# Kernel tuning notes

Hardware: AMD Instinct MI355X
Metric: run time of the kernel (lower is better)

Reference implementation:

```python
import jax, jax.numpy as jnp
import numpy as np

D_MODEL = 512
D_FFN = 2048
N_LAYERS = 6
VOCAB = 1000
D_STATE = 16
D_CONV = 4
D_INNER = 2 * D_MODEL  # expand=2
DT_RANK = 32           # ceil(d_model/16)
B, LT, LS = 2, 512, 512


def _pos_encoding(length, d_model):
    pos = np.arange(length, dtype=np.float32)[:, None]
    div = np.exp(np.arange(0, d_model, 2, dtype=np.float32) * (-np.log(10000.0) / d_model))
    pe = np.zeros((length, d_model), np.float32)
    pe[:, 0::2] = np.sin(pos * div)
    pe[:, 1::2] = np.cos(pos * div)
    return jnp.asarray(pe)


def _layer_norm(x, g, b, eps=1e-6):
    m = x.mean(-1, keepdims=True)
    v = ((x - m) ** 2).mean(-1, keepdims=True)
    return (x - m) * jax.lax.rsqrt(v + eps) * g + b


def _mamba(x, in_w, conv_w, conv_b, xproj_w, dt_w, dt_b, A_log, Dskip, out_w):
    # x: (b, l, d_model)
    b, l, _ = x.shape
    xz = x @ in_w.T                                   # (b, l, 2*d_inner)
    xc, z = jnp.split(xz, 2, axis=-1)
    # causal depthwise conv over time
    xt = jnp.transpose(xc, (0, 2, 1))                 # (b, d_inner, l)
    xt = jnp.pad(xt, ((0, 0), (0, 0), (D_CONV - 1, 0)))
    xt = jax.lax.conv_general_dilated(
        xt, conv_w, window_strides=(1,), padding='VALID',
        feature_group_count=D_INNER, dimension_numbers=('NCH', 'OIH', 'NCH'))
    xc = jax.nn.silu(jnp.transpose(xt, (0, 2, 1)) + conv_b)  # (b, l, d_inner)
    dbl = xc @ xproj_w.T                              # (b, l, dt_rank + 2*n)
    dt, Bm, Cm = jnp.split(dbl, [DT_RANK, DT_RANK + D_STATE], axis=-1)
    dt = jax.nn.softplus(dt @ dt_w.T + dt_b)          # (b, l, d_inner)
    A = -jnp.exp(A_log)                               # (d_inner, n)

    def step(h, xs):
        dt_t, B_t, C_t, u_t = xs                      # (b,d),(b,n),(b,n),(b,d)
        dA = jnp.exp(dt_t[..., None] * A)             # (b, d, n)
        h = dA * h + (dt_t * u_t)[..., None] * B_t[:, None, :]
        y = jnp.einsum('bdn,bn->bd', h, C_t)
        return h, y

    h0 = jnp.zeros((b, D_INNER, D_STATE), x.dtype)
    xs = (jnp.swapaxes(dt, 0, 1), jnp.swapaxes(Bm, 0, 1),
          jnp.swapaxes(Cm, 0, 1), jnp.swapaxes(xc, 0, 1))
    _, ys = jax.lax.scan(step, h0, xs)                # ys: (l, b, d_inner)
    y = jnp.swapaxes(ys, 0, 1) + xc * Dskip
    y = y * jax.nn.silu(z)
    return y @ out_w.T                                # (b, l, d_model)


def setup_inputs() -> dict:
    key = jax.random.key(0)
    ks = iter(jax.random.split(key, 40))

    def rn(shape, s=0.02):
        return jax.random.normal(next(ks), shape, jnp.float32) * s

    def mamba_params():
        return dict(
            in_w=rn((N_LAYERS, 2 * D_INNER, D_MODEL)),
            conv_w=rn((N_LAYERS, D_INNER, 1, D_CONV), 0.1),
            conv_b=rn((N_LAYERS, D_INNER)),
            xproj=rn((N_LAYERS, DT_RANK + 2 * D_STATE, D_INNER)),
            dtw=rn((N_LAYERS, D_INNER, DT_RANK)),
            dtb=rn((N_LAYERS, D_INNER)),
            Alog=jnp.log(jnp.broadcast_to(jnp.arange(1.0, D_STATE + 1.0, dtype=jnp.float32), (N_LAYERS, D_INNER, D_STATE))),
            D=jnp.ones((N_LAYERS, D_INNER), jnp.float32),
            outw=rn((N_LAYERS, D_MODEL, D_INNER)),
        )

    ps, pc = mamba_params(), mamba_params()
    inp = {
        'src': jax.random.normal(next(ks), (B, LS, D_MODEL), jnp.float32),
        'tgt': jax.random.randint(next(ks), (B, LT), 0, VOCAB),
        'emb': rn((VOCAB, D_MODEL)),
        'in_w_s': ps['in_w'], 'conv_w_s': ps['conv_w'], 'conv_b_s': ps['conv_b'],
        'xproj_s': ps['xproj'], 'dtw_s': ps['dtw'], 'dtb_s': ps['dtb'],
        'Alog_s': ps['Alog'], 'D_s': ps['D'], 'outw_s': ps['outw'],
        'in_w_c': pc['in_w'], 'conv_w_c': pc['conv_w'], 'conv_b_c': pc['conv_b'],
        'xproj_c': pc['xproj'], 'dtw_c': pc['dtw'], 'dtb_c': pc['dtb'],
        'Alog_c': pc['Alog'], 'D_c': pc['D'], 'outw_c': pc['outw'],
        'ffn_w1': rn((N_LAYERS, D_FFN, D_MODEL)),
        'ffn_b1': jnp.zeros((N_LAYERS, D_FFN), jnp.float32),
        'ffn_w2': rn((N_LAYERS, D_MODEL, D_FFN)),
        'ffn_b2': jnp.zeros((N_LAYERS, D_MODEL), jnp.float32),
        'ln_g': jnp.ones((N_LAYERS, 3, D_MODEL), jnp.float32),
        'ln_b': jnp.zeros((N_LAYERS, 3, D_MODEL), jnp.float32),
        'fin_g': jnp.ones((D_MODEL,), jnp.float32),
        'fin_b': jnp.zeros((D_MODEL,), jnp.float32),
    }
    return inp


def reference(src, tgt, emb, in_w_s, conv_w_s, conv_b_s, xproj_s, dtw_s, dtb_s,
              Alog_s, D_s, outw_s, in_w_c, conv_w_c, conv_b_c, xproj_c, dtw_c,
              dtb_c, Alog_c, D_c, outw_c, ffn_w1, ffn_b1, ffn_w2, ffn_b2,
              ln_g, ln_b, fin_g, fin_b):
    # NormalizedEmbedding + sinusoidal positional encoding
    x = emb[tgt] * jnp.sqrt(jnp.asarray(D_MODEL, jnp.float32))
    x = x + _pos_encoding(LT, D_MODEL)[None]
    for i in range(N_LAYERS):
        # self mamba (post-norm, normalize_before=False)
        t2 = _mamba(x, in_w_s[i], conv_w_s[i], conv_b_s[i], xproj_s[i],
                    dtw_s[i], dtb_s[i], Alog_s[i], D_s[i], outw_s[i])
        x = _layer_norm(x + t2, ln_g[i, 0], ln_b[i, 0])
        # cross mamba over concat([memory, tgt]) then take last LT steps
        cat = jnp.concatenate([src, x], axis=1)
        t2 = _mamba(cat, in_w_c[i], conv_w_c[i], conv_b_c[i], xproj_c[i],
                    dtw_c[i], dtb_c[i], Alog_c[i], D_c[i], outw_c[i])[:, -LT:]
        x = _layer_norm(x + t2, ln_g[i, 1], ln_b[i, 1])
        # positionwise FFN
        h = jax.nn.relu(x @ ffn_w1[i].T + ffn_b1[i]) @ ffn_w2[i].T + ffn_b2[i]
        x = _layer_norm(x + h, ln_g[i, 2], ln_b[i, 2])
    return _layer_norm(x, fin_g, fin_b)
```

## Files before the change

kernel.cpp:

```cpp
#include <hip/hip_runtime.h>
#include <math.h>

#define DMODEL 512
#define DINNER 1024
#define DSTATE 16
#define DTRANK 32
#define NLAYERS 6
#define BB 2
#define LT 512
#define LS 512

typedef __attribute__((ext_vector_type(8))) short bf16x8;
typedef __attribute__((ext_vector_type(8))) unsigned short u16x8;
typedef __attribute__((ext_vector_type(4))) float f32x4;

__device__ __forceinline__ unsigned short f2bf(float f) {
  unsigned u = __float_as_uint(f);
  u += 0x7fffu + ((u >> 16) & 1u);
  return (unsigned short)(u >> 16);
}
__device__ __forceinline__ float bf2f(unsigned short u) {
  return __uint_as_float((unsigned)u << 16);
}

template<int EPI>
__device__ __forceinline__ float epi_apply(float acc, float b) {
  if (EPI == 1) { float v = acc + b; return v > 0.f ? v : 0.f; }
  if (EPI == 2) { return acc + b; }
  if (EPI == 3) { float v = acc + b; return fmaxf(v, 0.f) + log1pf(__expf(-fabsf(v))); }
  return acc;
}

__global__ __launch_bounds__(256) void cvt_all_kernel(
    const float* __restrict__ i0, const float* __restrict__ i1,
    const float* __restrict__ i2, const float* __restrict__ i3,
    const float* __restrict__ i4, const float* __restrict__ i5,
    const float* __restrict__ i6, const float* __restrict__ i7,
    const float* __restrict__ i8, const float* __restrict__ i9,
    unsigned short* __restrict__ outbase) {
  int i = blockIdx.x * 256 + threadIdx.x;
  if (i >= 8159232) return;
  const float* in; int off;
  if      (i < 1572864) { in = i0; off = i; }
  else if (i < 3145728) { in = i1; off = i - 1572864; }
  else if (i < 3244032) { in = i2; off = i - 3145728; }
  else if (i < 3342336) { in = i3; off = i - 3244032; }
  else if (i < 3391488) { in = i4; off = i - 3342336; }
  else if (i < 3440640) { in = i5; off = i - 3391488; }
  else if (i < 4227072) { in = i6; off = i - 3440640; }
  else if (i < 5013504) { in = i7; off = i - 4227072; }
  else if (i < 6586368) { in = i8; off = i - 5013504; }
  else                  { in = i9; off = i - 6586368; }
  float4 a = ((const float4*)in)[off];
  ushort4 o = make_ushort4(f2bf(a.x), f2bf(a.y), f2bf(a.z), f2bf(a.w));
  *(ushort4*)&outbase[(size_t)i * 4] = o;
}

__global__ __launch_bounds__(256) void embed_kernel(const int* __restrict__ tgt,
    const float* __restrict__ emb, float* __restrict__ X,
    unsigned short* __restrict__ Xb) {
  int i = blockIdx.x * 256 + threadIdx.x;
  int d = i & (DMODEL - 1);
  int bt = i >> 9;
  int t = bt & (LT - 1);
  int tok = tgt[bt];
  float div = __expf((float)(d & ~1) * (-9.210340371976184f / (float)DMODEL));
  float ang = (float)t * div;
  float pe = (d & 1) ? cosf(ang) : sinf(ang);
  float v = emb[(size_t)tok * DMODEL + d] * 22.627416997969522f + pe;
  X[i] = v;
  Xb[i] = f2bf(v);
}

__global__ __launch_bounds__(256) void catsrc_kernel(const float* __restrict__ src,
    unsigned short* __restrict__ CATb) {
  int i = blockIdx.x * 256 + threadIdx.x;
  int c8 = (i & 63) * 8;
  int r = i >> 6;
  int b = r >> 9, l = r & 511;
  const float* s = src + ((size_t)b * 512 + l) * DMODEL + c8;
  float4 a = *(const float4*)s;
  float4 bq = *(const float4*)(s + 4);
  u16x8 o;
  o[0] = f2bf(a.x); o[1] = f2bf(a.y); o[2] = f2bf(a.z); o[3] = f2bf(a.w);
  o[4] = f2bf(bq.x); o[5] = f2bf(bq.y); o[6] = f2bf(bq.z); o[7] = f2bf(bq.w);
  *(u16x8*)&CATb[((size_t)b * 1024 + l) * DMODEL + c8] = o;
}

template<int BK, int EPI, bool SPLIT, bool OUTB>
__global__ __launch_bounds__(256) void mgemmA(
    const unsigned short* __restrict__ A, const unsigned short* __restrict__ Bw,
    const float* __restrict__ bias, float* __restrict__ C,
    unsigned short* __restrict__ Cb, int M, int N, int K, int lda) {
  constexpr int PAD = BK + 8;
  constexpr int CHA = BK / 32;
  constexpr int CHB = BK / 16;
  __shared__ __align__(16) unsigned short As[64 * PAD];
  __shared__ __align__(16) unsigned short Bs[128 * PAD];
  const int tid = threadIdx.x;
  const int bn = blockIdx.x * 128;
  const int bm = blockIdx.y * 64;
  const int lane = tid & 63;
  const int w = tid >> 6;
  const int wr = (w >> 1) * 32;
  const int wc = (w & 1) * 64;
  const int l15 = lane & 15;
  const int l4 = lane >> 4;
  const int koff = l4 * 8;
  int kcnt = K, kbeg = 0;
  if (SPLIT) { kcnt = K / (int)gridDim.z; kbeg = blockIdx.z * kcnt; }
  const int nt = kcnt / BK;
  f32x4 acc[2][4] = {};

  int arow_[CHA], ak8_[CHA];
  const unsigned short* Ap[CHA];
#pragma unroll
  for (int i = 0; i < CHA; ++i) {
    int f = tid + 256 * i;
    arow_[i] = f / (BK / 8);
    ak8_[i] = (f % (BK / 8)) * 8;
    Ap[i] = A + (size_t)(bm + arow_[i]) * lda + kbeg + ak8_[i];
  }
  int brow_[CHB], bk8_[CHB];
  const unsigned short* Bp[CHB];
#pragma unroll
  for (int i = 0; i < CHB; ++i) {
    int f = tid + 256 * i;
    brow_[i] = f / (BK / 8);
    bk8_[i] = (f % (BK / 8)) * 8;
    Bp[i] = Bw + (size_t)(bn + brow_[i]) * K + kbeg + bk8_[i];
  }

  u16x8 av[CHA], bv[CHB];
#pragma unroll
  for (int i = 0; i < CHA; ++i) av[i] = *(const u16x8*)Ap[i];
#pragma unroll
  for (int i = 0; i < CHB; ++i) bv[i] = *(const u16x8*)Bp[i];

  for (int t = 0; t < nt; ++t) {
    __syncthreads();
#pragma unroll
    for (int i = 0; i < CHA; ++i) *(u16x8*)&As[arow_[i] * PAD + ak8_[i]] = av[i];
#pragma unroll
    for (int i = 0; i < CHB; ++i) *(u16x8*)&Bs[brow_[i] * PAD + bk8_[i]] = bv[i];
    if (t + 1 < nt) {
      int ko = (t + 1) * BK;
#pragma unroll
      for (int i = 0; i < CHA; ++i) av[i] = *(const u16x8*)(Ap[i] + ko);
#pragma unroll
      for (int i = 0; i < CHB; ++i) bv[i] = *(const u16x8*)(Bp[i] + ko);
    }
    __syncthreads();
#pragma unroll
    for (int kk = 0; kk < BK / 32; ++kk) {
      bf16x8 afr[2], bfr[4];
#pragma unroll
      for (int i = 0; i < 2; ++i)
        afr[i] = *(const bf16x8*)&As[(wr + i * 16 + l15) * PAD + kk * 32 + koff];
#pragma unroll
      for (int j = 0; j < 4; ++j)
        bfr[j] = *(const bf16x8*)&Bs[(wc + j * 16 + l15) * PAD + kk * 32 + koff];
#pragma unroll
      for (int fr = 0; fr < 2; ++fr)
#pragma unroll
        for (int fc = 0; fc < 4; ++fc)
          acc[fr][fc] = __builtin_amdgcn_mfma_f32_16x16x32_bf16(
              afr[fr], bfr[fc], acc[fr][fc], 0, 0, 0);
    }
  }

  if (SPLIT) {
    float* Pz = C + (size_t)blockIdx.z * M * N;
#pragma unroll
    for (int fc = 0; fc < 4; ++fc) {
      int col = bn + wc + fc * 16 + l15;
#pragma unroll
      for (int fr = 0; fr < 2; ++fr) {
        int row0 = bm + wr + fr * 16 + l4 * 4;
#pragma unroll
        for (int r = 0; r < 4; ++r)
          Pz[(size_t)(row0 + r) * N + col] = acc[fr][fc][r];
      }
    }
  } else {
#pragma unroll
    for (int fc = 0; fc < 4; ++fc) {
      int col = bn + wc + fc * 16 + l15;
      float bvs = (EPI != 0) ? bias[col] : 0.f;
#pragma unroll
      for (int fr = 0; fr < 2; ++fr) {
        int row0 = bm + wr + fr * 16 + l4 * 4;
#pragma unroll
        for (int r = 0; r < 4; ++r) {
          float v = epi_apply<EPI>(acc[fr][fc][r], bvs);
          if (OUTB) Cb[(size_t)(row0 + r) * N + col] = f2bf(v);
          else      C[(size_t)(row0 + r) * N + col] = v;
        }
      }
    }
  }
}

template<int BK, int EPI, bool SPLIT, bool OUTB>
__global__ __launch_bounds__(256) void mgemm(
    const unsigned short* __restrict__ A, const unsigned short* __restrict__ Bw,
    const float* __restrict__ bias, float* __restrict__ C,
    unsigned short* __restrict__ Cb, int M, int N, int K, int lda) {
  constexpr int PAD = BK + 8;
  constexpr int CH = BK / 32;
  __shared__ __align__(16) unsigned short As[64 * PAD];
  __shared__ __align__(16) unsigned short Bs[64 * PAD];
  const int tid = threadIdx.x;
  const int bn = blockIdx.x * 64;
  const int bm = blockIdx.y * 64;
  const int lane = tid & 63;
  const int w = tid >> 6;
  const int wr = (w >> 1) * 32;
  const int wc = (w & 1) * 32;
  const int l15 = lane & 15;
  const int l4 = lane >> 4;
  const int koff = l4 * 8;
  int kcnt = K, kbeg = 0;
  if (SPLIT) { kcnt = K / (int)gridDim.z; kbeg = blockIdx.z * kcnt; }
  const int nt = kcnt / BK;
  f32x4 acc[2][2] = {};

  int row_[CH], k8_[CH];
  const unsigned short *Ap[CH], *Bp[CH];
#pragma unroll
  for (int i = 0; i < CH; ++i) {
    int f = tid + 256 * i;
    row_[i] = f / (BK / 8);
    k8_[i] = (f % (BK / 8)) * 8;
    Ap[i] = A + (size_t)(bm + row_[i]) * lda + kbeg + k8_[i];
    Bp[i] = Bw + (size_t)(bn + row_[i]) * K + kbeg + k8_[i];
  }

  u16x8 av[CH], bv[CH];
#pragma unroll
  for (int i = 0; i < CH; ++i) { av[i] = *(const u16x8*)Ap[i]; bv[i] = *(const u16x8*)Bp[i]; }

  for (int t = 0; t < nt; ++t) {
    __syncthreads();
#pragma unroll
    for (int i = 0; i < CH; ++i) {
      *(u16x8*)&As[row_[i] * PAD + k8_[i]] = av[i];
      *(u16x8*)&Bs[row_[i] * PAD + k8_[i]] = bv[i];
    }
    if (t + 1 < nt) {
      int ko = (t + 1) * BK;
#pragma unroll
      for (int i = 0; i < CH; ++i) {
        av[i] = *(const u16x8*)(Ap[i] + ko);
        bv[i] = *(const u16x8*)(Bp[i] + ko);
      }
    }
    __syncthreads();
#pragma unroll
    for (int kk = 0; kk < CH; ++kk) {
      bf16x8 afr[2], bfr[2];
#pragma unroll
      for (int i = 0; i < 2; ++i) {
        afr[i] = *(const bf16x8*)&As[(wr + i * 16 + l15) * PAD + kk * 32 + koff];
        bfr[i] = *(const bf16x8*)&Bs[(wc + i * 16 + l15) * PAD + kk * 32 + koff];
      }
#pragma unroll
      for (int fr = 0; fr < 2; ++fr)
#pragma unroll
        for (int fc = 0; fc < 2; ++fc)
          acc[fr][fc] = __builtin_amdgcn_mfma_f32_16x16x32_bf16(
              afr[fr], bfr[fc], acc[fr][fc], 0, 0, 0);
    }
  }

  if (SPLIT) {
    float* Pz = C + (size_t)blockIdx.z * M * N;
#pragma unroll
    for (int fc = 0; fc < 2; ++fc) {
      int col = bn + wc + fc * 16 + l15;
#pragma unroll
      for (int fr = 0; fr < 2; ++fr) {
        int row0 = bm + wr + fr * 16 + l4 * 4;
#pragma unroll
        for (int r = 0; r < 4; ++r)
          Pz[(size_t)(row0 + r) * N + col] = acc[fr][fc][r];
      }
    }
  } else {
#pragma unroll
    for (int fc = 0; fc < 2; ++fc) {
      int col = bn + wc + fc * 16 + l15;
      float bvs = (EPI != 0) ? bias[col] : 0.f;
#pragma unroll
      for (int fr = 0; fr < 2; ++fr) {
        int row0 = bm + wr + fr * 16 + l4 * 4;
#pragma unroll
        for (int r = 0; r < 4; ++r) {
          float v = epi_apply<EPI>(acc[fr][fc][r], bvs);
          if (OUTB) Cb[(size_t)(row0 + r) * N + col] = f2bf(v);
          else      C[(size_t)(row0 + r) * N + col] = v;
        }
      }
    }
  }
}

__global__ __launch_bounds__(256) void mgemm_dt(
    const float* __restrict__ XPP, const unsigned short* __restrict__ Bw,
    const float* __restrict__ bias, unsigned short* __restrict__ Cb,
    int M, int N) {
  constexpr int PAD = 40;
  __shared__ __align__(16) unsigned short As[64 * PAD];
  __shared__ __align__(16) unsigned short Bs[64 * PAD];
  const int tid = threadIdx.x;
  const int bn = blockIdx.x * 64;
  const int bm = blockIdx.y * 64;
  const int lane = tid & 63;
  const int w = tid >> 6;
  const int wr = (w >> 1) * 32;
  const int wc = (w & 1) * 32;
  const int l15 = lane & 15;
  const int l4 = lane >> 4;
  const int koff = l4 * 8;
  const size_t zs = (size_t)M * 64;
  {
    int r = tid >> 2, c8 = (tid & 3) * 8;
    const float* p = XPP + (size_t)(bm + r) * 64 + c8;
    float s[8] = {0.f, 0.f, 0.f, 0.f, 0.f, 0.f, 0.f, 0.f};
#pragma unroll
    for (int z = 0; z < 8; ++z) {
      float4 a = *(const float4*)(p + z * zs);
      float4 b = *(const float4*)(p + z * zs + 4);
      s[0] += a.x; s[1] += a.y; s[2] += a.z; s[3] += a.w;
      s[4] += b.x; s[5] += b.y; s[6] += b.z; s[7] += b.w;
    }
    u16x8 o;
#pragma unroll
    for (int j = 0; j < 8; ++j) o[j] = f2bf(s[j]);
    *(u16x8*)&As[r * PAD + c8] = o;
    *(u16x8*)&Bs[r * PAD + c8] = *(const u16x8*)(Bw + (size_t)(bn + r) * 32 + c8);
  }
  __syncthreads();
  bf16x8 afr[2], bfr[2];
#pragma unroll
  for (int i = 0; i < 2; ++i) {
    afr[i] = *(const bf16x8*)&As[(wr + i * 16 + l15) * PAD + koff];
    bfr[i] = *(const bf16x8*)&Bs[(wc + i * 16 + l15) * PAD + koff];
  }
  f32x4 acc[2][2] = {};
#pragma unroll
  for (int fr = 0; fr < 2; ++fr)
#pragma unroll
    for (int fc = 0; fc < 2; ++fc)
      acc[fr][fc] = __builtin_amdgcn_mfma_f32_16x16x32_bf16(
          afr[fr], bfr[fc], acc[fr][fc], 0, 0, 0);
#pragma unroll
  for (int fc = 0; fc < 2; ++fc) {
    int col = bn + wc + fc * 16 + l15;
    float bvs = bias[col];
#pragma unroll
    for (int fr = 0; fr < 2; ++fr) {
      int row0 = bm + wr + fr * 16 + l4 * 4;
#pragma unroll
      for (int r = 0; r < 4; ++r)
        Cb[(size_t)(row0 + r) * N + col] = f2bf(epi_apply<3>(acc[fr][fc][r], bvs));
    }
  }
}

__global__ __launch_bounds__(256) void conv_silu_kernel(
    const unsigned short* __restrict__ xzb, const float* __restrict__ w,
    const float* __restrict__ bias, unsigned short* __restrict__ outb, int L) {
  int idx = blockIdx.x * 256 + threadIdx.x;
  int d8 = (idx & 127) * 8;
  int bt = idx >> 7;
  int b = bt / L;
  int t = bt - b * L;
  const unsigned short* col = xzb + ((size_t)b * L) * (2 * DINNER) + d8;
  float acc[8];
  float4 wv[8];
#pragma unroll
  for (int j = 0; j < 8; ++j) {
    acc[j] = bias[d8 + j];
    wv[j] = *(const float4*)(w + (size_t)(d8 + j) * 4);
  }
#pragma unroll
  for (int k = 0; k < 4; ++k) {
    int tt = t - 3 + k;
    if (tt >= 0) {
      u16x8 v = *(const u16x8*)(col + (size_t)tt * (2 * DINNER));
      float wk[8] = {
        k == 0 ? wv[0].x : k == 1 ? wv[0].y : k == 2 ? wv[0].z : wv[0].w,
        k == 0 ? wv[1].x : k == 1 ? wv[1].y : k == 2 ? wv[1].z : wv[1].w,
        k == 0 ? wv[2].x : k == 1 ? wv[2].y : k == 2 ? wv[2].z : wv[2].w,
        k == 0 ? wv[3].x : k == 1 ? wv[3].y : k == 2 ? wv[3].z : wv[3].w,
        k == 0 ? wv[4].x : k == 1 ? wv[4].y : k == 2 ? wv[4].z : wv[4].w,
        k == 0 ? wv[5].x : k == 1 ? wv[5].y : k == 2 ? wv[5].z : wv[5].w,
        k == 0 ? wv[6].x : k == 1 ? wv[6].y : k == 2 ? wv[6].z : wv[6].w,
        k == 0 ? wv[7].x : k == 1 ? wv[7].y : k == 2 ? wv[7].z : wv[7].w };
#pragma unroll
      for (int j = 0; j < 8; ++j) acc[j] = fmaf(bf2f(v[j]), wk[j], acc[j]);
    }
  }
  u16x8 o;
#pragma unroll
  for (int j = 0; j < 8; ++j) {
    float sig = 1.f / (1.f + __expf(-acc[j]));
    o[j] = f2bf(acc[j] * sig);
  }
  *(u16x8*)&outb[(size_t)bt * DINNER + d8] = o;
}

__global__ __launch_bounds__(256) void scan_pass1(
    const unsigned short* __restrict__ dt, const float* __restrict__ XPP,
    const unsigned short* __restrict__ u, const float* __restrict__ Alog,
    float* __restrict__ P, float* __restrict__ S, int L, int CL) {
  __shared__ float BC[32][32];
  const int tid = threadIdx.x;
  const int d = blockIdx.x * 256 + tid;
  const int b = blockIdx.y;
  const int c = blockIdx.z;
  const int t0 = c * CL;
  if (tid < CL * 4) {
    int t = tid >> 2, j8 = (tid & 3) * 8;
    const float* p = XPP + ((size_t)b * L + t0 + t) * 64 + 32 + j8;
    const size_t zs = (size_t)BB * L * 64;
    float s[8] = {0.f, 0.f, 0.f, 0.f, 0.f, 0.f, 0.f, 0.f};
#pragma unroll
    for (int z = 0; z < 8; ++z) {
      float4 a = *(const float4*)(p + z * zs);
      float4 bq = *(const float4*)(p + z * zs + 4);
      s[0] += a.x; s[1] += a.y; s[2] += a.z; s[3] += a.w;
      s[4] += bq.x; s[5] += bq.y; s[6] += bq.z; s[7] += bq.w;
    }
#pragma unroll
    for (int j = 0; j < 8; ++j) BC[t][j8 + j] = s[j];
  }
  float A[16], h[16], Pp[16];
#pragma unroll
  for (int j = 0; j < 4; ++j) {
    float4 a4 = *(const float4*)(Alog + d * 16 + j * 4);
    A[j * 4 + 0] = -__expf(a4.x); A[j * 4 + 1] = -__expf(a4.y);
    A[j * 4 + 2] = -__expf(a4.z); A[j * 4 + 3] = -__expf(a4.w);
  }
#pragma unroll
  for (int n = 0; n < 16; ++n) { h[n] = 0.f; Pp[n] = 1.f; }
  const unsigned short* dtp = dt + ((size_t)b * L + t0) * DINNER + d;
  const unsigned short* up  = u  + ((size_t)b * L + t0) * DINNER + d;
  __syncthreads();
  float dtv = bf2f(dtp[0]), uv = bf2f(up[0]);
  for (int t = 0; t < CL; ++t) {
    float dtn = 0.f, un = 0.f;
    if (t + 1 < CL) {
      dtn = bf2f(dtp[(size_t)(t + 1) * DINNER]);
      un  = bf2f(up[(size_t)(t + 1) * DINNER]);
    }
    float du = dtv * uv;
#pragma unroll
    for (int n = 0; n < 16; ++n) {
      float dA = __expf(dtv * A[n]);
      Pp[n] *= dA;
      h[n] = fmaf(dA, h[n], du * BC[t][n]);
    }
    dtv = dtn; uv = un;
  }
  size_t base = (size_t)c * 32768 + ((size_t)(b * 1024 + d) << 4);
#pragma unroll
  for (int j = 0; j < 4; ++j) {
    *(float4*)&P[base + j * 4] = make_float4(Pp[j*4], Pp[j*4+1], Pp[j*4+2], Pp[j*4+3]);
    *(float4*)&S[base + j * 4] = make_float4(h[j*4], h[j*4+1], h[j*4+2], h[j*4+3]);
  }
}

__global__ __launch_bounds__(256) void scan_pass2(
    const unsigned short* __restrict__ dt, const float* __restrict__ XPP,
    const unsigned short* __restrict__ u, const unsigned short* __restrict__ xzb,
    const float* __restrict__ Alog, const float* __restrict__ Dsk,
    const float* __restrict__ P, const float* __restrict__ S,
    unsigned short* __restrict__ ysb, int L, int CL, int c0) {
  __shared__ float BC[32][32];
  const int tid = threadIdx.x;
  const int d = blockIdx.x * 256 + tid;
  const int b = blockIdx.y;
  const int c = blockIdx.z + c0;
  const int t0 = c * CL;
  if (tid < CL * 4) {
    int t = tid >> 2, j8 = (tid & 3) * 8;
    const float* p = XPP + ((size_t)b * L + t0 + t) * 64 + 32 + j8;
    const size_t zs = (size_t)BB * L * 64;
    float s[8] = {0.f, 0.f, 0.f, 0.f, 0.f, 0.f, 0.f, 0.f};
#pragma unroll
    for (int z = 0; z < 8; ++z) {
      float4 a = *(const float4*)(p + z * zs);
      float4 bq = *(const float4*)(p + z * zs + 4);
      s[0] += a.x; s[1] += a.y; s[2] += a.z; s[3] += a.w;
      s[4] += bq.x; s[5] += bq.y; s[6] += bq.z; s[7] += bq.w;
    }
#pragma unroll
    for (int j = 0; j < 8; ++j) BC[t][j8 + j] = s[j];
  }
  float A[16], h[16];
#pragma unroll
  for (int j = 0; j < 4; ++j) {
    float4 a4 = *(const float4*)(Alog + d * 16 + j * 4);
    A[j * 4 + 0] = -__expf(a4.x); A[j * 4 + 1] = -__expf(a4.y);
    A[j * 4 + 2] = -__expf(a4.z); A[j * 4 + 3] = -__expf(a4.w);
  }
#pragma unroll
  for (int n = 0; n < 16; ++n) h[n] = 0.f;
  size_t sbase = (size_t)(b * 1024 + d) << 4;
  for (int cc = 0; cc < c; ++cc) {
    size_t bb = (size_t)cc * 32768 + sbase;
#pragma unroll
    for (int j = 0; j < 4; ++j) {
      float4 p4 = *(const float4*)&P[bb + j * 4];
      float4 s4 = *(const float4*)&S[bb + j * 4];
      h[j*4+0] = fmaf(p4.x, h[j*4+0], s4.x);
      h[j*4+1] = fmaf(p4.y, h[j*4+1], s4.y);
      h[j*4+2] = fmaf(p4.z, h[j*4+2], s4.z);
      h[j*4+3] = fmaf(p4.w, h[j*4+3], s4.w);
    }
  }
  float Dv = Dsk[d];
  const unsigned short* dtp = dt + ((size_t)b * L + t0) * DINNER + d;
  const unsigned short* up  = u  + ((size_t)b * L + t0) * DINNER + d;
  const unsigned short* zp  = xzb + ((size_t)b * L + t0) * (2 * DINNER) + DINNER + d;
  unsigned short* yp = ysb + ((size_t)(b * 512) + (t0 - c0 * CL)) * DINNER + d;
  __syncthreads();
  float dtv = bf2f(dtp[0]), uv = bf2f(up[0]), zv = bf2f(zp[0]);
  for (int t = 0; t < CL; ++t) {
    float dtn = 0.f, un = 0.f, zn = 0.f;
    if (t + 1 < CL) {
      dtn = bf2f(dtp[(size_t)(t + 1) * DINNER]);
      un  = bf2f(up[(size_t)(t + 1) * DINNER]);
      zn  = bf2f(zp[(size_t)(t + 1) * (2 * DINNER)]);
    }
    float du = dtv * uv;
    float y = 0.f;
#pragma unroll
    for (int n = 0; n < 16; ++n) {
      float dA = __expf(dtv * A[n]);
      h[n] = fmaf(dA, h[n], du * BC[t][n]);
      y = fmaf(h[n], BC[t][16 + n], y);
    }
    float sig = 1.f / (1.f + __expf(-zv));
    yp[(size_t)t * DINNER] = f2bf((y + uv * Dv) * (zv * sig));
    dtv = dtn; uv = un; zv = zn;
  }
}

template<int NZ, int EPI>
__global__ __launch_bounds__(64) void ln_red_kernel(
    const float* __restrict__ res, const float* __restrict__ P,
    const float* __restrict__ bias, const float* __restrict__ g,
    const float* __restrict__ be, float* __restrict__ out,
    unsigned short* __restrict__ outb, int row_scale, int row_off) {
  int r = blockIdx.x;
  int b = r >> 9, t = r & 511;
  int lane = threadIdx.x;
  const float* rp = res + (size_t)r * DMODEL;
  size_t ob = ((size_t)(b * row_scale + row_off + t)) * DMODEL;
  float v[8];
  float s = 0.f, ss = 0.f;
#pragma unroll
  for (int j = 0; j < 8; ++j) {
    int col = lane + j * 64;
    float acc = 0.f;
#pragma unroll
    for (int z = 0; z < NZ; ++z) acc += P[(size_t)z * 524288 + (size_t)r * DMODEL + col];
    float bv = (EPI != 0) ? bias[col] : 0.f;
    float x = rp[col] + epi_apply<EPI>(acc, bv);
    v[j] = x; s += x; ss += x * x;
  }
#pragma unroll
  for (int o = 32; o > 0; o >>= 1) { s += __shfl_xor(s, o); ss += __shfl_xor(ss, o); }
  float m = s * (1.f / 512.f);
  float var = ss * (1.f / 512.f) - m * m;
  float rs = rsqrtf(var + 1e-6f);
#pragma unroll
  for (int j = 0; j < 8; ++j) {
    int col = lane + j * 64;
    float o2 = (v[j] - m) * rs * g[col] + be[col];
    out[(size_t)r * DMODEL + col] = o2;
    outb[ob + col] = f2bf(o2);
  }
}

__global__ __launch_bounds__(64) void ln_final_kernel(
    const float* __restrict__ res, const float* __restrict__ g,
    const float* __restrict__ be, float* __restrict__ out) {
  int r = blockIdx.x;
  int lane = threadIdx.x;
  const float* rp = res + (size_t)r * DMODEL;
  float v[8];
  float s = 0.f, ss = 0.f;
#pragma unroll
  for (int j = 0; j < 8; ++j) {
    float x = rp[lane + j * 64];
    v[j] = x; s += x; ss += x * x;
  }
#pragma unroll
  for (int o = 32; o > 0; o >>= 1) { s += __shfl_xor(s, o); ss += __shfl_xor(ss, o); }
  float m = s * (1.f / 512.f);
  float var = ss * (1.f / 512.f) - m * m;
  float rs = rsqrtf(var + 1e-6f);
#pragma unroll
  for (int j = 0; j < 8; ++j) {
    int c = lane + j * 64;
    out[(size_t)r * DMODEL + c] = (v[j] - m) * rs * g[c] + be[c];
  }
}

extern "C" void kernel_launch(void* const* d_in, const int* in_sizes, int n_in,
                              void* d_out, int out_size, void* d_ws, size_t ws_size,
                              hipStream_t stream) {
  (void)in_sizes; (void)n_in; (void)out_size; (void)ws_size;
  const float* src      = (const float*)d_in[0];
  const int*   tgt      = (const int*)d_in[1];
  const float* emb      = (const float*)d_in[2];
  const float* in_w_s   = (const float*)d_in[3];
  const float* conv_w_s = (const float*)d_in[4];
  const float* conv_b_s = (const float*)d_in[5];
  const float* xproj_s  = (const float*)d_in[6];
  const float* dtw_s    = (const float*)d_in[7];
  const float* dtb_s    = (const float*)d_in[8];
  const float* Alog_s   = (const float*)d_in[9];
  const float* D_s      = (const float*)d_in[10];
  const float* outw_s   = (const float*)d_in[11];
  const float* in_w_c   = (const float*)d_in[12];
  const float* conv_w_c = (const float*)d_in[13];
  const float* conv_b_c = (const float*)d_in[14];
  const float* xproj_c  = (const float*)d_in[15];
  const float* dtw_c    = (const float*)d_in[16];
  const float* dtb_c    = (const float*)d_in[17];
  const float* Alog_c   = (const float*)d_in[18];
  const float* D_c      = (const float*)d_in[19];
  const float* outw_c   = (const float*)d_in[20];
  const float* ffn_w1   = (const float*)d_in[21];
  const float* ffn_b1   = (const float*)d_in[22];
  const float* ffn_w2   = (const float*)d_in[23];
  const float* ffn_b2   = (const float*)d_in[24];
  const float* ln_g     = (const float*)d_in[25];
  const float* ln_b     = (const float*)d_in[26];
  const float* fin_g    = (const float*)d_in[27];
  const float* fin_b    = (const float*)d_in[28];

  float* ws   = (float*)d_ws;
  float* X    = ws;
  float* XZ   = X + 524288;
  float* XPP  = XZ + 4194304;
  float* SC_P = XPP + 1048576;
  float* SC_S = SC_P + 1048576;
  unsigned short* U = (unsigned short*)(SC_S + 1048576);
  unsigned short* Xb   = U;
  unsigned short* CATb = Xb + 524288;
  unsigned short* XCb  = CATb + 1048576;
  unsigned short* XZb  = XCb + 2097152;
  unsigned short* YSb  = XZb + 4194304;
  unsigned short* DTb  = YSb + 1048576;
  unsigned short* WB   = DTb + 2097152;
  unsigned short* inwsb = WB;
  unsigned short* inwcb = inwsb + 6291456;
  unsigned short* xpsb  = inwcb + 6291456;
  unsigned short* xpcb  = xpsb + 393216;
  unsigned short* dtwsb = xpcb + 393216;
  unsigned short* dtwcb = dtwsb + 196608;
  unsigned short* owsb  = dtwcb + 196608;
  unsigned short* owcb  = owsb + 3145728;
  unsigned short* f1b   = owcb + 3145728;
  unsigned short* f2b   = f1b + 6291456;

  cvt_all_kernel<<<31872, 256, 0, stream>>>(
      in_w_s, in_w_c, xproj_s, xproj_c, dtw_s, dtw_c, outw_s, outw_c,
      ffn_w1, ffn_w2, WB);
  embed_kernel<<<2048, 256, 0, stream>>>(tgt, emb, X, Xb);
  catsrc_kernel<<<256, 256, 0, stream>>>(src, CATb);

  for (int i = 0; i < NLAYERS; ++i) {
    mgemmA<64, 0, false, true><<<dim3(16, 16), 256, 0, stream>>>(
        Xb, inwsb + (size_t)i * 1048576, nullptr, nullptr, XZb, 1024, 2048, 512, 512);
    conv_silu_kernel<<<512, 256, 0, stream>>>(
        XZb, conv_w_s + (size_t)i * 4096, conv_b_s + (size_t)i * 1024, XCb, 512);
    mgemm<64, 0, true, false><<<dim3(1, 16, 8), 256, 0, stream>>>(
        XCb, xpsb + (size_t)i * 65536, nullptr, XPP, nullptr, 1024, 64, 1024, 1024);
    mgemm_dt<<<dim3(16, 16), 256, 0, stream>>>(
        XPP, dtwsb + (size_t)i * 32768, dtb_s + (size_t)i * 1024, DTb, 1024, 1024);
    scan_pass1<<<dim3(4, 2, 32), 256, 0, stream>>>(
        DTb, XPP, XCb, Alog_s + (size_t)i * 16384, SC_P, SC_S, 512, 16);
    scan_pass2<<<dim3(4, 2, 32), 256, 0, stream>>>(
        DTb, XPP, XCb, XZb, Alog_s + (size_t)i * 16384, D_s + (size_t)i * 1024,
        SC_P, SC_S, YSb, 512, 16, 0);
    mgemmA<64, 0, true, false><<<dim3(4, 16, 4), 256, 0, stream>>>(
        YSb, owsb + (size_t)i * 524288, nullptr, XZ, nullptr, 1024, 512, 1024, 1024);
    ln_red_kernel<4, 0><<<1024, 64, 0, stream>>>(
        X, XZ, nullptr, ln_g + (size_t)(i * 3 + 0) * 512,
        ln_b + (size_t)(i * 3 + 0) * 512, X, CATb, 1024, 512);

    mgemmA<64, 0, false, true><<<dim3(16, 32), 256, 0, stream>>>(
        CATb, inwcb + (size_t)i * 1048576, nullptr, nullptr, XZb, 2048, 2048, 512, 512);
    conv_silu_kernel<<<1024, 256, 0, stream>>>(
        XZb, conv_w_c + (size_t)i * 4096, conv_b_c + (size_t)i * 1024, XCb, 1024);
    mgemm<64, 0, true, false><<<dim3(1, 32, 8), 256, 0, stream>>>(
        XCb, xpcb + (size_t)i * 65536, nullptr, XPP, nullptr, 2048, 64, 1024, 1024);
    mgemm_dt<<<dim3(16, 32), 256, 0, stream>>>(
        XPP, dtwcb + (size_t)i * 32768, dtb_c + (size_t)i * 1024, DTb, 2048, 1024);
    scan_pass1<<<dim3(4, 2, 32), 256, 0, stream>>>(
        DTb, XPP, XCb, Alog_c + (size_t)i * 16384, SC_P, SC_S, 1024, 32);
    scan_pass2<<<dim3(4, 2, 16), 256, 0, stream>>>(
        DTb, XPP, XCb, XZb, Alog_c + (size_t)i * 16384, D_c + (size_t)i * 1024,
        SC_P, SC_S, YSb, 1024, 32, 16);
    mgemmA<64, 0, true, false><<<dim3(4, 16, 4), 256, 0, stream>>>(
        YSb, owcb + (size_t)i * 524288, nullptr, XZ, nullptr, 1024, 512, 1024, 1024);
    ln_red_kernel<4, 0><<<1024, 64, 0, stream>>>(
        X, XZ, nullptr, ln_g + (size_t)(i * 3 + 1) * 512,
        ln_b + (size_t)(i * 3 + 1) * 512, X, Xb, 512, 0);

    mgemmA<64, 1, false, true><<<dim3(16, 16), 256, 0, stream>>>(
        Xb, f1b + (size_t)i * 1048576, ffn_b1 + (size_t)i * 2048, nullptr, XZb,
        1024, 2048, 512, 512);
    mgemmA<64, 0, true, false><<<dim3(4, 16, 8), 256, 0, stream>>>(
        XZb, f2b + (size_t)i * 1048576, nullptr, XZ, nullptr, 1024, 512, 2048, 2048);
    ln_red_kernel<8, 2><<<1024, 64, 0, stream>>>(
        X, XZ, ffn_b2 + (size_t)i * 512, ln_g + (size_t)(i * 3 + 2) * 512,
        ln_b + (size_t)(i * 3 + 2) * 512, X, Xb, 512, 0);
  }

  ln_final_kernel<<<1024, 64, 0, stream>>>(X, fin_g, fin_b, (float*)d_out);
}
```

Measured before the change: 1.194 ms.

## Fuse two-pass chunked scan with flag-based inter-block sync; retune GEMM launches

After: 2.401 ms. 2.01x slower.

```diff
diff --git a/kernel.cpp b/kernel.cpp
--- a/kernel.cpp
+++ b/kernel.cpp
@@ -9,6 +9,7 @@
 #define BB 2
 #define LT 512
 #define LS 512
+#define NC 32
 
 typedef __attribute__((ext_vector_type(8))) short bf16x8;
 typedef __attribute__((ext_vector_type(8))) unsigned short u16x8;
@@ -411,13 +412,16 @@
   *(u16x8*)&outb[(size_t)bt * DINNER + d8] = o;
 }
 
-__global__ __launch_bounds__(256) void scan_pass1(
+__global__ __launch_bounds__(256) void scan_fused(
     const unsigned short* __restrict__ dt, const float* __restrict__ XPP,
-    const unsigned short* __restrict__ u, const float* __restrict__ Alog,
-    float* __restrict__ P, float* __restrict__ S, int L, int CL) {
+    const unsigned short* __restrict__ u, const unsigned short* __restrict__ xzb,
+    const float* __restrict__ Alog, const float* __restrict__ Dsk,
+    float* __restrict__ P, float* __restrict__ S, int* __restrict__ flags,
+    unsigned short* __restrict__ ysb, int L, int CL, int c0y) {
   __shared__ float BC[32][32];
   const int tid = threadIdx.x;
-  const int d = blockIdx.x * 256 + tid;
+  const int dblk = blockIdx.x;
+  const int d = dblk * 256 + tid;
   const int b = blockIdx.y;
   const int c = blockIdx.z;
   const int t0 = c * CL;
@@ -436,80 +440,62 @@
 #pragma unroll
     for (int j = 0; j < 8; ++j) BC[t][j8 + j] = s[j];
   }
-  float A[16], h[16], Pp[16];
+  float A[16];
 #pragma unroll
   for (int j = 0; j < 4; ++j) {
     float4 a4 = *(const float4*)(Alog + d * 16 + j * 4);
     A[j * 4 + 0] = -__expf(a4.x); A[j * 4 + 1] = -__expf(a4.y);
     A[j * 4 + 2] = -__expf(a4.z); A[j * 4 + 3] = -__expf(a4.w);
   }
-#pragma unroll
-  for (int n = 0; n < 16; ++n) { h[n] = 0.f; Pp[n] = 1.f; }
   const unsigned short* dtp = dt + ((size_t)b * L + t0) * DINNER + d;
   const unsigned short* up  = u  + ((size_t)b * L + t0) * DINNER + d;
   __syncthreads();
-  float dtv = bf2f(dtp[0]), uv = bf2f(up[0]);
-  for (int t = 0; t < CL; ++t) {
-    float dtn = 0.f, un = 0.f;
-    if (t + 1 < CL) {
-      dtn = bf2f(dtp[(size_t)(t + 1) * DINNER]);
-      un  = bf2f(up[(size_t)(t + 1) * DINNER]);
-    }
-    float du = dtv * uv;
-#pragma unroll
-    for (int n = 0; n < 16; ++n) {
-      float dA = __expf(dtv * A[n]);
-      Pp[n] *= dA;
-      h[n] = fmaf(dA, h[n], du * BC[t][n]);
-    }
-    dtv = dtn; uv = un;
+
+  float h[16];
+#pragma unroll
+  for (int n = 0; n < 16; ++n) h[n] = 0.f;
+  float sdt = 0.f;
+  {
+    float dtv = bf2f(dtp[0]), uv = bf2f(up[0]);
+    for (int t = 0; t < CL; ++t) {
+      float dtn = 0.f, un = 0.f;
+      if (t + 1 < CL) {
+        dtn = bf2f(dtp[(size_t)(t + 1) * DINNER]);
+        un  = bf2f(up[(size_t)(t + 1) * DINNER]);
+      }
+      sdt += dtv;
+      float du = dtv * uv;
+#pragma unroll
+      for (int n = 0; n < 16; ++n)
+        h[n] = fmaf(__expf(dtv * A[n]), h[n], du * BC[t][n]);
+      dtv = dtn; uv = un;
+    }
   }
   size_t base = (size_t)c * 32768 + ((size_t)(b * 1024 + d) << 4);
 #pragma unroll
   for (int j = 0; j < 4; ++j) {
-    *(float4*)&P[base + j * 4] = make_float4(Pp[j*4], Pp[j*4+1], Pp[j*4+2], Pp[j*4+3]);
+    float4 p4 = make_float4(__expf(sdt * A[j*4]), __expf(sdt * A[j*4+1]),
+                            __expf(sdt * A[j*4+2]), __expf(sdt * A[j*4+3]));
+    *(float4*)&P[base + j * 4] = p4;
     *(float4*)&S[base + j * 4] = make_float4(h[j*4], h[j*4+1], h[j*4+2], h[j*4+3]);
   }
-}
-
-__global__ __launch_bounds__(256) void scan_pass2(
-    const unsigned short* __restrict__ dt, const float* __restrict__ XPP,
-    const unsigned short* __restrict__ u, const unsigned short* __restrict__ xzb,
-    const float* __restrict__ Alog, const float* __restrict__ Dsk,
-    const float* __restrict__ P, const float* __restrict__ S,
-    unsigned short* __restrict__ ysb, int L, int CL, int c0) {
-  __shared__ float BC[32][32];
-  const int tid = threadIdx.x;
-  const int d = blockIdx.x * 256 + tid;
-  const int b = blockIdx.y;
-  const int c = blockIdx.z + c0;
-  const int t0 = c * CL;
-  if (tid < CL * 4) {
-    int t = tid >> 2, j8 = (tid & 3) * 8;
-    const float* p = XPP + ((size_t)b * L + t0 + t) * 64 + 32 + j8;
-    const size_t zs = (size_t)BB * L * 64;
-    float s[8] = {0.f, 0.f, 0.f, 0.f, 0.f, 0.f, 0.f, 0.f};
-#pragma unroll
-    for (int z = 0; z < 8; ++z) {
-      float4 a = *(const float4*)(p + z * zs);
-      float4 bq = *(const float4*)(p + z * zs + 4);
-      s[0] += a.x; s[1] += a.y; s[2] += a.z; s[3] += a.w;
-      s[4] += bq.x; s[5] += bq.y; s[6] += bq.z; s[7] += bq.w;
-    }
-#pragma unroll
-    for (int j = 0; j < 8; ++j) BC[t][j8 + j] = s[j];
-  }
-  float A[16], h[16];
-#pragma unroll
-  for (int j = 0; j < 4; ++j) {
-    float4 a4 = *(const float4*)(Alog + d * 16 + j * 4);
-    A[j * 4 + 0] = -__expf(a4.x); A[j * 4 + 1] = -__expf(a4.y);
-    A[j * 4 + 2] = -__expf(a4.z); A[j * 4 + 3] = -__expf(a4.w);
-  }
+  __threadfence();
+  __syncthreads();
+  const int fbase = (b * 4 + dblk) * NC;
+  if (tid == 0) atomicExch(&flags[fbase + c], 1);
+
+  if (c < c0y) return;
+
 #pragma unroll
   for (int n = 0; n < 16; ++n) h[n] = 0.f;
   size_t sbase = (size_t)(b * 1024 + d) << 4;
   for (int cc = 0; cc < c; ++cc) {
+    if (tid == 0) {
+      while (atomicAdd(&flags[fbase + cc], 0) == 0) {}
+    }
+    __syncthreads();
+    if (tid == 0) __threadfence();
+    __syncthreads();
     size_t bb = (size_t)cc * 32768 + sbase;
 #pragma unroll
     for (int j = 0; j < 4; ++j) {
@@ -521,12 +507,10 @@
       h[j*4+3] = fmaf(p4.w, h[j*4+3], s4.w);
     }
   }
+
   float Dv = Dsk[d];
-  const unsigned short* dtp = dt + ((size_t)b * L + t0) * DINNER + d;
-  const unsigned short* up  = u  + ((size_t)b * L + t0) * DINNER + d;
-  const unsigned short* zp  = xzb + ((size_t)b * L + t0) * (2 * DINNER) + DINNER + d;
-  unsigned short* yp = ysb + ((size_t)(b * 512) + (t0 - c0 * CL)) * DINNER + d;
-  __syncthreads();
+  const unsigned short* zp = xzb + ((size_t)b * L + t0) * (2 * DINNER) + DINNER + d;
+  unsigned short* yp = ysb + ((size_t)(b * 512) + (t0 - c0y * CL)) * DINNER + d;
   float dtv = bf2f(dtp[0]), uv = bf2f(up[0]), zv = bf2f(zp[0]);
   for (int t = 0; t < CL; ++t) {
     float dtn = 0.f, un = 0.f, zn = 0.f;
@@ -669,15 +653,18 @@
   unsigned short* owcb  = owsb + 3145728;
   unsigned short* f1b   = owcb + 3145728;
   unsigned short* f2b   = f1b + 6291456;
-
+  int* flags = (int*)(f2b + 6291456);
+
+  hipMemsetAsync(flags, 0, 12 * 256 * sizeof(int), stream);
   cvt_all_kernel<<<31872, 256, 0, stream>>>(
       in_w_s, in_w_c, xproj_s, xproj_c, dtw_s, dtw_c, outw_s, outw_c,
       ffn_w1, ffn_w2, WB);
   embed_kernel<<<2048, 256, 0, stream>>>(tgt, emb, X, Xb);
   catsrc_kernel<<<256, 256, 0, stream>>>(src, CATb);
 
+  int inst = 0;
   for (int i = 0; i < NLAYERS; ++i) {
-    mgemmA<64, 0, false, true><<<dim3(16, 16), 256, 0, stream>>>(
+    mgemm<64, 0, false, true><<<dim3(32, 16), 256, 0, stream>>>(
         Xb, inwsb + (size_t)i * 1048576, nullptr, nullptr, XZb, 1024, 2048, 512, 512);
     conv_silu_kernel<<<512, 256, 0, stream>>>(
         XZb, conv_w_s + (size_t)i * 4096, conv_b_s + (size_t)i * 1024, XCb, 512);
@@ -685,14 +672,13 @@
         XCb, xpsb + (size_t)i * 65536, nullptr, XPP, nullptr, 1024, 64, 1024, 1024);
     mgemm_dt<<<dim3(16, 16), 256, 0, stream>>>(
         XPP, dtwsb + (size_t)i * 32768, dtb_s + (size_t)i * 1024, DTb, 1024, 1024);
-    scan_pass1<<<dim3(4, 2, 32), 256, 0, stream>>>(
-        DTb, XPP, XCb, Alog_s + (size_t)i * 16384, SC_P, SC_S, 512, 16);
-    scan_pass2<<<dim3(4, 2, 32), 256, 0, stream>>>(
+    scan_fused<<<dim3(4, 2, NC), 256, 0, stream>>>(
         DTb, XPP, XCb, XZb, Alog_s + (size_t)i * 16384, D_s + (size_t)i * 1024,
-        SC_P, SC_S, YSb, 512, 16, 0);
-    mgemmA<64, 0, true, false><<<dim3(4, 16, 4), 256, 0, stream>>>(
+        SC_P, SC_S, flags + inst * 256, YSb, 512, 16, 0);
+    inst++;
+    mgemmA<64, 0, true, false><<<dim3(4, 16, 8), 256, 0, stream>>>(
         YSb, owsb + (size_t)i * 524288, nullptr, XZ, nullptr, 1024, 512, 1024, 1024);
-    ln_red_kernel<4, 0><<<1024, 64, 0, stream>>>(
+    ln_red_kernel<8, 0><<<1024, 64, 0, stream>>>(
         X, XZ, nullptr, ln_g + (size_t)(i * 3 + 0) * 512,
         ln_b + (size_t)(i * 3 + 0) * 512, X, CATb, 1024, 512);
 
@@ -704,18 +690,17 @@
         XCb, xpcb + (size_t)i * 65536, nullptr, XPP, nullptr, 2048, 64, 1024, 1024);
     mgemm_dt<<<dim3(16, 32), 256, 0, stream>>>(
         XPP, dtwcb + (size_t)i * 32768, dtb_c + (size_t)i * 1024, DTb, 2048, 1024);
-    scan_pass1<<<dim3(4, 2, 32), 256, 0, stream>>>(
-        DTb, XPP, XCb, Alog_c + (size_t)i * 16384, SC_P, SC_S, 1024, 32);
-    scan_pass2<<<dim3(4, 2, 16), 256, 0, stream>>>(
+    scan_fused<<<dim3(4, 2, NC), 256, 0, stream>>>(
         DTb, XPP, XCb, XZb, Alog_c + (size_t)i * 16384, D_c + (size_t)i * 1024,
-        SC_P, SC_S, YSb, 1024, 32, 16);
-    mgemmA<64, 0, true, false><<<dim3(4, 16, 4), 256, 0, stream>>>(
+        SC_P, SC_S, flags + inst * 256, YSb, 1024, 32, 16);
+    inst++;
+    mgemmA<64, 0, true, false><<<dim3(4, 16, 8), 256, 0, stream>>>(
         YSb, owcb + (size_t)i * 524288, nullptr, XZ, nullptr, 1024, 512, 1024, 1024);
-    ln_red_kernel<4, 0><<<1024, 64, 0, stream>>>(
+    ln_red_kernel<8, 0><<<1024, 64, 0, stream>>>(
         X, XZ, nullptr, ln_g + (size_t)(i * 3 + 1) * 512,
         ln_b + (size_t)(i * 3 + 1) * 512, X, Xb, 512, 0);
 
-    mgemmA<64, 1, false, true><<<dim3(16, 16), 256, 0, stream>>>(
+    mgemm<64, 1, false, true><<<dim3(32, 16), 256, 0, stream>>>(
         Xb, f1b + (size_t)i * 1048576, ffn_b1 + (size_t)i * 2048, nullptr, XZb,
         1024, 2048, 512, 512);
     mgemmA<64, 0, true, false><<<dim3(4, 16, 8), 256, 0, stream>>>(
```
